# Optimization experiments

Hardware: AMD Instinct MI355X
Metric: run time of the kernel (lower is better)

Reference implementation:

```python
import jax, jax.numpy as jnp
import numpy as np
import math

EMBED_DIM = 1024
N_HEADS = 16
HEAD_DIM = EMBED_DIM // N_HEADS
NUM_FEATURES = 32
R_NODES = 2
EPS = 1e-06
C_CONST = 2.0 + EPS
CHUNK = 512


def setup_inputs() -> dict:
    key = jax.random.key(0)
    ks = jax.random.split(key, 8)
    B, T = 2, 4096
    x = jax.random.normal(ks[0], (B, T, EMBED_DIM), dtype=jnp.float32)
    w_qkv = jax.random.normal(ks[1], (3 * EMBED_DIM, EMBED_DIM), dtype=jnp.float32) * 0.02
    b_qkv = jnp.zeros((3 * EMBED_DIM,), dtype=jnp.float32)
    w_out = jax.random.normal(ks[2], (EMBED_DIM, EMBED_DIM), dtype=jnp.float32) * 0.02
    b_out = jnp.zeros((EMBED_DIM,), dtype=jnp.float32)
    omega = jax.random.normal(ks[3], (R_NODES, N_HEADS, HEAD_DIM, NUM_FEATURES), dtype=jnp.float32)
    nodes, weights = np.polynomial.laguerre.laggauss(R_NODES)
    quad_nodes = jnp.asarray(nodes, dtype=jnp.float32) / C_CONST
    quad_weights = jnp.asarray(weights, dtype=jnp.float32) / C_CONST
    return {"x": x, "w_qkv": w_qkv, "b_qkv": b_qkv, "w_out": w_out,
            "b_out": b_out, "omega": omega, "quad_nodes": quad_nodes,
            "quad_weights": quad_weights}


def _compute_features(z, omega, quad_nodes, quad_weights):
    # z: [B,H,T,D] -> fused features [B,H,T,R*M]
    R, M = omega.shape[0], omega.shape[-1]
    nrm = jnp.linalg.norm(z, axis=-1, keepdims=True)
    zn = z / jnp.maximum(nrm, 1e-12)  # F.normalize
    proj = jnp.einsum('bhtd,rhdm->rbhtm', zn, omega)
    inv_sqrt_m = 1.0 / math.sqrt(M)
    poly = (proj ** 2) * inv_sqrt_m
    s = quad_nodes.reshape(R, 1, 1, 1, 1)
    sqrt_2s = jnp.sqrt(2.0 * jnp.maximum(quad_nodes, 0.0)).reshape(R, 1, 1, 1, 1)
    exp_arg = jnp.clip(proj * sqrt_2s - s, -20.0, 20.0)
    prf = jnp.exp(exp_arg) * inv_sqrt_m
    sqw = jnp.sqrt(jnp.maximum(quad_weights, 0.0)).reshape(R, 1, 1, 1, 1)
    fused = poly * prf * sqw  # [R,B,H,T,M]
    B, H, T = z.shape[0], z.shape[1], z.shape[2]
    return jnp.transpose(fused, (1, 2, 3, 0, 4)).reshape(B, H, T, R * M)


def _forward(x, w_qkv, b_qkv, w_out, b_out, omega, quad_nodes, quad_weights):
    B, T, C = x.shape
    H, D = N_HEADS, HEAD_DIM
    qkv = x @ w_qkv.T + b_qkv  # [B,T,3C]
    q, k, v = jnp.split(qkv, 3, axis=-1)
    def to_bhtd(t):
        return jnp.transpose(t.reshape(B, T, H, D), (0, 2, 1, 3)).astype(jnp.float32)
    q, k, v = to_bhtd(q), to_bhtd(k), to_bhtd(v)
    qf = _compute_features(q, omega, quad_nodes, quad_weights)  # [B,H,T,F]
    kf = _compute_features(k, omega, quad_nodes, quad_weights)
    F_dim = qf.shape[-1]
    nc = T // CHUNK
    # chunked causal linear attention via scan over chunks
    def to_chunks(t):  # [B,H,T,...] -> [nc,B,H,CHUNK,...]
        new_shape = (t.shape[0], t.shape[1], nc, CHUNK) + t.shape[3:]
        return jnp.moveaxis(t.reshape(new_shape), 2, 0)
    qf_c, kf_c, v_c = to_chunks(qf), to_chunks(kf), to_chunks(v)

    kv0 = jnp.zeros((B, H, F_dim, D), dtype=jnp.float32)
    k0 = jnp.zeros((B, H, F_dim), dtype=jnp.float32)

    def step(carry, inp):
        kv_s, k_s = carry
        qc, kc, vc = inp
        kv_prod = jnp.einsum('bhtf,bhtd->bhtfd', kc, vc)
        kv_cum = jnp.cumsum(kv_prod, axis=2) + kv_s[:, :, None]
        k_cum = jnp.cumsum(kc, axis=2) + k_s[:, :, None]
        ctx = jnp.einsum('bhtf,bhtfd->bhtd', qc, kv_cum)
        den = jnp.maximum(jnp.einsum('bhtf,bhtf->bht', qc, k_cum), 1e-06)
        out_c = ctx / den[..., None]
        return (kv_cum[:, :, -1], k_cum[:, :, -1]), out_c

    _, out_chunks = jax.lax.scan(step, (kv0, k0), (qf_c, kf_c, v_c))
    out = jnp.moveaxis(out_chunks, 0, 2).reshape(B, H, T, D)  # [B,H,T,D]
    out = jnp.transpose(out, (0, 2, 1, 3)).reshape(B, T, C)
    return out @ w_out.T + b_out


def reference(x, w_qkv, b_qkv, w_out, b_out, omega, quad_nodes, quad_weights):
    return _forward(x, w_qkv, b_qkv, w_out, b_out, omega, quad_nodes, quad_weights)
```

## Files before the change

kernel.cpp:

```cpp
#include <hip/hip_runtime.h>
#include <math.h>

#define EMBED   1024
#define THREEC  3072
#define NH      16
#define HD      64
#define NFEAT   64
#define RN      2
#define MM_     32
#define B_      2
#define T_      4096
#define L_      64
#define NC_     64
#define BH_     32

typedef __attribute__((ext_vector_type(8))) short bf16x8;
typedef __attribute__((ext_vector_type(4))) short bf16x4;
typedef __attribute__((ext_vector_type(4))) float f32x4;

__device__ __forceinline__ float bf2f(short s) {
    unsigned u = ((unsigned)(unsigned short)s) << 16;
    return __builtin_bit_cast(float, u);
}
__device__ __forceinline__ short f2bf(float f) {
    unsigned u = __builtin_bit_cast(unsigned, f);
    u += 0x7fff + ((u >> 16) & 1);
    return (short)(u >> 16);
}
__device__ __forceinline__ void gload16(const short* g, short* l) {
    __builtin_amdgcn_global_load_lds(
        (const __attribute__((address_space(1))) void*)g,
        (__attribute__((address_space(3))) void*)l, 16, 0, 0);
}

#define NV_X   1048576
#define NV_WQ  393216
#define NV_WO  131072
#define NV_ALL (NV_X + NV_WQ + NV_WO)
__global__ __launch_bounds__(256) void prep_kernel(
    const float* __restrict__ x, const float* __restrict__ wq,
    const float* __restrict__ wo, const float* __restrict__ omega,
    short* __restrict__ xb, short* __restrict__ wqb, short* __restrict__ wob,
    short* __restrict__ omgH, short* __restrict__ omgL)
{
    int i = blockIdx.x * 256 + threadIdx.x;
    if (i < NV_ALL) {
        const float* src; short* dst; int k;
        if (i < NV_X)            { src = x;  dst = xb;  k = i; }
        else if (i < NV_X+NV_WQ) { src = wq; dst = wqb; k = i - NV_X; }
        else                     { src = wo; dst = wob; k = i - NV_X - NV_WQ; }
        const float4* p = (const float4*)src + (size_t)k * 2;
        float4 a = p[0], b = p[1];
        bf16x8 o = { f2bf(a.x), f2bf(a.y), f2bf(a.z), f2bf(a.w),
                     f2bf(b.x), f2bf(b.y), f2bf(b.z), f2bf(b.w) };
        *((bf16x8*)dst + k) = o;
    } else {
        int j = i - NV_ALL;
        if (j < NH * NFEAT * HD) {
            int d = j & 63;
            int f = (j >> 6) & 63;
            int h = j >> 12;
            int r = f >> 5, m = f & 31;
            float w = omega[(((size_t)(r * NH + h) * HD + d) * MM_) + m];
            short a = f2bf(w);
            omgH[j] = a;
            omgL[j] = f2bf(w - bf2f(a));
        }
    }
}

template<int OUTBF>
__global__ __launch_bounds__(256) void gemm_bf16(
    const short* __restrict__ A,
    const short* __restrict__ W,
    const float* __restrict__ bias,
    float* __restrict__ Cf, short* __restrict__ Cb,
    int M, int N, int K)
{
    __shared__ short lA[2][128 * 32];
    __shared__ short lB[2][128 * 32];
    const int tid  = threadIdx.x;
    const int nbn  = N >> 7;
    const int cpx  = gridDim.x >> 3;
    const int swz  = (blockIdx.x & 7) * cpx + (blockIdx.x >> 3);
    const int bm   = (swz / nbn) << 7;
    const int bn   = (swz % nbn) << 7;
    const int lane = tid & 63;
    const int wave = tid >> 6;
    const int row0 = (wave >> 1) * 64;
    const int col0 = (wave & 1) * 64;
    const int lr   = lane & 15;
    const int kg8  = (lane >> 4) * 8;

    f32x4 acc[4][4] = {};

#define STAGE(buf, k0)                                                        \
    {                                                                         \
        _Pragma("unroll")                                                     \
        for (int i = 0; i < 2; ++i) {                                         \
            int idx = i * 256 + tid;                                          \
            int row = idx >> 2, kq = (idx & 3) * 8;                           \
            gload16(&A[(size_t)(bm + row) * K + (k0) + kq], &lA[buf][idx * 8]); \
            gload16(&W[(size_t)(bn + row) * K + (k0) + kq], &lB[buf][idx * 8]); \
        }                                                                     \
    }

    const int KT = K >> 5;
    STAGE(0, 0);
    __syncthreads();
    int cur = 0;
    for (int kt = 0; kt < KT; ++kt) {
        if (kt + 1 < KT) STAGE(cur ^ 1, (kt + 1) * 32);
        const short* As = lA[cur];
        const short* Bs = lB[cur];
        bf16x8 af[4], bfr[4];
        #pragma unroll
        for (int m = 0; m < 4; ++m)
            af[m] = *(const bf16x8*)&As[(row0 + m * 16 + lr) * 32 + kg8];
        #pragma unroll
        for (int n = 0; n < 4; ++n)
            bfr[n] = *(const bf16x8*)&Bs[(col0 + n * 16 + lr) * 32 + kg8];
        #pragma unroll
        for (int m = 0; m < 4; ++m)
            #pragma unroll
            for (int n = 0; n < 4; ++n)
                acc[m][n] = __builtin_amdgcn_mfma_f32_16x16x32_bf16(
                    af[m], bfr[n], acc[m][n], 0, 0, 0);
        __syncthreads();
        cur ^= 1;
    }
#undef STAGE

    #pragma unroll
    for (int n = 0; n < 4; ++n) {
        const int col = bn + col0 + n * 16 + (lane & 15);
        const float bvv = bias[col];
        #pragma unroll
        for (int m = 0; m < 4; ++m) {
            const int rbase = bm + row0 + m * 16 + (lane >> 4) * 4;
            #pragma unroll
            for (int j = 0; j < 4; ++j) {
                const float v = acc[m][n][j] + bvv;
                if (OUTBF) Cb[(size_t)(rbase + j) * N + col] = f2bf(v);
                else       Cf[(size_t)(rbase + j) * N + col] = v;
            }
        }
    }
}

__global__ __launch_bounds__(256) void feat_fused(
    const short* __restrict__ qkvb,
    const short* __restrict__ omgH,
    const short* __restrict__ omgL,
    const float* __restrict__ qn,
    const float* __restrict__ qw,
    short* __restrict__ qf,
    short* __restrict__ ctxb,
    float* __restrict__ rs_g,
    short* __restrict__ cKVb,
    float* __restrict__ cK)
{
    __shared__ short zq[64][72];
    __shared__ short zk[64][72];
    __shared__ short omh[64][72];
    __shared__ short oml[64][72];
    __shared__ float invn[2][64];
    __shared__ float rs_l[64];

    const int tid   = threadIdx.x;
    const int chunk = blockIdx.x;
    const int bh    = chunk >> 6;
    const int c     = chunk & 63;
    const int b     = bh >> 4, h = bh & 15;
    const int t0    = c * 64;

    {
        const int row = tid >> 2;
        const int c0  = (tid & 3) * 16;
        const size_t zbase = ((size_t)(b * T_ + t0 + row)) * THREEC + h * HD + c0;
        const size_t obase = ((size_t)h * NFEAT + row) * HD + c0;
        *(bf16x8*)&zq[row][c0]      = *(const bf16x8*)&qkvb[zbase];
        *(bf16x8*)&zq[row][c0 + 8]  = *(const bf16x8*)&qkvb[zbase + 8];
        *(bf16x8*)&zk[row][c0]      = *(const bf16x8*)&qkvb[zbase + EMBED];
        *(bf16x8*)&zk[row][c0 + 8]  = *(const bf16x8*)&qkvb[zbase + EMBED + 8];
        *(bf16x8*)&omh[row][c0]     = *(const bf16x8*)&omgH[obase];
        *(bf16x8*)&omh[row][c0 + 8] = *(const bf16x8*)&omgH[obase + 8];
        *(bf16x8*)&oml[row][c0]     = *(const bf16x8*)&omgL[obase];
        *(bf16x8*)&oml[row][c0 + 8] = *(const bf16x8*)&omgL[obase + 8];
    }
    __syncthreads();

    {
        const int t = tid >> 2;
        const int q = tid & 3;
        #pragma unroll
        for (int p = 0; p < 2; ++p) {
            const short* Z = p ? &zk[t][q * 16] : &zq[t][q * 16];
            float ss = 0.0f;
            #pragma unroll
            for (int j = 0; j < 16; ++j) { float v = bf2f(Z[j]); ss += v * v; }
            ss += __shfl_xor(ss, 1, 64);
            ss += __shfl_xor(ss, 2, 64);
            if (q == 0) invn[p][t] = 1.0f / fmaxf(sqrtf(ss), 1e-12f);
        }
    }
    __syncthreads();

    const int wave = tid >> 6;
    const int lane = tid & 63;
    const int p    = wave >> 1;
    const int half = wave & 1;
    const short (*Z)[72] = p ? zk : zq;

    const float s0 = qn[0], s1 = qn[1];
    const float sq2s0 = sqrtf(2.0f * fmaxf(s0, 0.0f));
    const float sq2s1 = sqrtf(2.0f * fmaxf(s1, 0.0f));
    const float sc0 = sqrtf(fmaxf(qw[0], 0.0f)) * (1.0f / 32.0f);
    const float sc1 = sqrtf(fmaxf(qw[1], 0.0f)) * (1.0f / 32.0f);

    const int lr  = lane & 15;
    const int G   = lane >> 4;
    const int kg8 = G * 8;

    f32x4 acc[2][4] = {};
    #pragma unroll
    for (int kk = 0; kk < 2; ++kk) {
        bf16x8 a[2], bh8[4], bl8[4];
        #pragma unroll
        for (int m = 0; m < 2; ++m)
            a[m] = *(const bf16x8*)&Z[half * 32 + m * 16 + lr][kk * 32 + kg8];
        #pragma unroll
        for (int n = 0; n < 4; ++n) {
            bh8[n] = *(const bf16x8*)&omh[n * 16 + lr][kk * 32 + kg8];
            bl8[n] = *(const bf16x8*)&oml[n * 16 + lr][kk * 32 + kg8];
        }
        #pragma unroll
        for (int m = 0; m < 2; ++m)
            #pragma unroll
            for (int n = 0; n < 4; ++n) {
                acc[m][n] = __builtin_amdgcn_mfma_f32_16x16x32_bf16(
                    a[m], bh8[n], acc[m][n], 0, 0, 0);
                acc[m][n] = __builtin_amdgcn_mfma_f32_16x16x32_bf16(
                    a[m], bl8[n], acc[m][n], 0, 0, 0);
            }
    }
    __syncthreads();

    short (*kfT)[72] = zq;
    short (*vT)[72]  = zk;
    short (*Qrm)[72] = omh;
    short (*Krm)[72] = oml;
    {
        #pragma unroll
        for (int n = 0; n < 4; ++n) {
            const int f = n * 16 + lr;
            const float s_r   = (n < 2) ? s0 : s1;
            const float sq2s  = (n < 2) ? sq2s0 : sq2s1;
            const float scale = (n < 2) ? sc0 : sc1;
            #pragma unroll
            for (int m = 0; m < 2; ++m) {
                const int tb4 = half * 32 + m * 16 + G * 4;
                #pragma unroll
                for (int j = 0; j < 4; ++j) {
                    const int t = tb4 + j;
                    const float proj = acc[m][n][j] * invn[p][t];
                    const float arg = fminf(fmaxf(proj * sq2s - s_r, -20.0f), 20.0f);
                    const float val = proj * proj * __expf(arg) * scale;
                    const short vb  = f2bf(val);
                    if (p == 0) { Qrm[t][f] = vb; }
                    else        { kfT[f][t] = vb; Krm[t][f] = vb; }
                }
            }
        }
    }
    {
        const int row = tid >> 2;
        const int c0  = (tid & 3) * 16;
        const short* vrow = qkvb + ((size_t)(b * T_ + t0 + row)) * THREEC
                          + 2 * EMBED + h * HD;
        bf16x8 v0 = *(const bf16x8*)&vrow[c0], v1 = *(const bf16x8*)&vrow[c0 + 8];
        #pragma unroll
        for (int j = 0; j < 8; ++j) {
            vT[c0 + j][row]     = v0[j];
            vT[c0 + 8 + j][row] = v1[j];
        }
    }
    __syncthreads();

    const int r0 = wave * 16;

    {
        const int row = tid >> 2;
        const int c0  = (tid & 3) * 16;
        short* dst = qf + ((size_t)bh * T_ + t0 + row) * NFEAT;
        *(bf16x8*)&dst[c0]     = *(const bf16x8*)&Qrm[row][c0];
        *(bf16x8*)&dst[c0 + 8] = *(const bf16x8*)&Qrm[row][c0 + 8];
    }
    bf16x8 aqq[2];
    aqq[0] = *(const bf16x8*)&Qrm[r0 + lr][kg8];
    aqq[1] = *(const bf16x8*)&Qrm[r0 + lr][32 + kg8];
    f32x4 accA[4] = {};
    #pragma unroll
    for (int n = 0; n < 4; ++n) {
        accA[n] = __builtin_amdgcn_mfma_f32_16x16x32_bf16(
            aqq[0], *(const bf16x8*)&Krm[n * 16 + lr][kg8], accA[n], 0, 0, 0);
        accA[n] = __builtin_amdgcn_mfma_f32_16x16x32_bf16(
            aqq[1], *(const bf16x8*)&Krm[n * 16 + lr][32 + kg8], accA[n], 0, 0, 0);
    }
    {
        float rsum[4] = {0.0f, 0.0f, 0.0f, 0.0f};
        #pragma unroll
        for (int n = 0; n < 4; ++n) {
            const int s = n * 16 + lr;
            #pragma unroll
            for (int j = 0; j < 4; ++j) {
                const int t = r0 + G * 4 + j;
                if (s <= t) rsum[j] += accA[n][j];
            }
        }
        #pragma unroll
        for (int j = 0; j < 4; ++j) {
            rsum[j] += __shfl_xor(rsum[j], 1, 64);
            rsum[j] += __shfl_xor(rsum[j], 2, 64);
            rsum[j] += __shfl_xor(rsum[j], 4, 64);
            rsum[j] += __shfl_xor(rsum[j], 8, 64);
        }
        if (lr == 0) {
            #pragma unroll
            for (int j = 0; j < 4; ++j) rs_l[r0 + G * 4 + j] = rsum[j];
        }
    }
    {
        bf16x8 a2[2];
        a2[0] = *(const bf16x8*)&kfT[wave * 16 + lr][kg8];
        a2[1] = *(const bf16x8*)&kfT[wave * 16 + lr][32 + kg8];
        f32x4 sa[4] = {};
        #pragma unroll
        for (int n = 0; n < 4; ++n) {
            sa[n] = __builtin_amdgcn_mfma_f32_16x16x32_bf16(
                a2[0], *(const bf16x8*)&vT[n * 16 + lr][kg8], sa[n], 0, 0, 0);
            sa[n] = __builtin_amdgcn_mfma_f32_16x16x32_bf16(
                a2[1], *(const bf16x8*)&vT[n * 16 + lr][32 + kg8], sa[n], 0, 0, 0);
        }
        short* basep = cKVb + (size_t)chunk * (NFEAT * HD);
        #pragma unroll
        for (int n = 0; n < 4; ++n) {
            bf16x4 o = { f2bf(sa[n][0]), f2bf(sa[n][1]),
                         f2bf(sa[n][2]), f2bf(sa[n][3]) };
            *(bf16x4*)&basep[(n * 16 + lr) * NFEAT + wave * 16 + G * 4] = o;
        }
    }
    {
        const int f  = tid >> 2;
        const int tq = tid & 3;
        float s = 0.0f;
        #pragma unroll
        for (int j = 0; j < 16; ++j) s += bf2f(kfT[f][tq * 16 + j]);
        s += __shfl_xor(s, 1, 64);
        s += __shfl_xor(s, 2, 64);
        if (tq == 0) cK[(size_t)chunk * NFEAT + f] = s;
    }
    __syncthreads();

    short (*At)[72] = oml;
    #pragma unroll
    for (int n = 0; n < 4; ++n) {
        const int s = n * 16 + lr;
        #pragma unroll
        for (int j = 0; j < 4; ++j) {
            const int t = r0 + G * 4 + j;
            At[t][s] = f2bf((s <= t) ? accA[n][j] : 0.0f);
        }
    }
    __syncthreads();

    {
        bf16x8 aa[2];
        aa[0] = *(const bf16x8*)&At[r0 + lr][kg8];
        aa[1] = *(const bf16x8*)&At[r0 + lr][32 + kg8];
        f32x4 a2[4] = {};
        #pragma unroll
        for (int n = 0; n < 4; ++n) {
            a2[n] = __builtin_amdgcn_mfma_f32_16x16x32_bf16(
                aa[0], *(const bf16x8*)&vT[n * 16 + lr][kg8], a2[n], 0, 0, 0);
            a2[n] = __builtin_amdgcn_mfma_f32_16x16x32_bf16(
                aa[1], *(const bf16x8*)&vT[n * 16 + lr][32 + kg8], a2[n], 0, 0, 0);
        }
        #pragma unroll
        for (int n = 0; n < 4; ++n) {
            const int d = n * 16 + lr;
            #pragma unroll
            for (int j = 0; j < 4; ++j) {
                const int t = r0 + G * 4 + j;
                At[t][d] = f2bf(a2[n][j]);
            }
        }
    }
    __syncthreads();
    {
        const int row = tid >> 2;
        const int c0  = (tid & 3) * 16;
        short* dst = ctxb + ((size_t)bh * T_ + t0 + row) * NFEAT;
        *(bf16x8*)&dst[c0]     = *(const bf16x8*)&At[row][c0];
        *(bf16x8*)&dst[c0 + 8] = *(const bf16x8*)&At[row][c0 + 8];
    }
    if (tid < 64) rs_g[(size_t)bh * T_ + t0 + tid] = rs_l[tid];
}

__global__ __launch_bounds__(256) void prefix_scan(
    short* __restrict__ cKVb, float* __restrict__ cK)
{
    const int bh  = blockIdx.x >> 2;
    const int sl  = blockIdx.x & 3;
    const int tid = threadIdx.x;
    short* base = cKVb + (size_t)bh * NC_ * (NFEAT * HD) + sl * 1024 + tid * 4;
    bf16x4 n0 = *(const bf16x4*)(base);
    bf16x4 n1 = *(const bf16x4*)(base + 4096);
    float pref[4] = {0.0f, 0.0f, 0.0f, 0.0f};
    for (int c = 0; c < NC_; ++c) {
        bf16x4 cur = n0;
        n0 = n1;
        if (c + 2 < NC_) n1 = *(const bf16x4*)(base + (size_t)(c + 2) * 4096);
        else { n1[0] = 0; n1[1] = 0; n1[2] = 0; n1[3] = 0; }
        bf16x4 o = { f2bf(pref[0]), f2bf(pref[1]), f2bf(pref[2]), f2bf(pref[3]) };
        *(bf16x4*)(base + (size_t)c * 4096) = o;
        pref[0] += bf2f(cur[0]); pref[1] += bf2f(cur[1]);
        pref[2] += bf2f(cur[2]); pref[3] += bf2f(cur[3]);
    }
    if (sl == 0 && tid < 64) {
        float* kb = cK + (size_t)bh * NC_ * NFEAT + tid;
        float m0 = kb[0];
        float m1 = kb[64];
        float p = 0.0f;
        for (int c = 0; c < NC_; ++c) {
            float cu = m0;
            m0 = m1;
            m1 = (c + 2 < NC_) ? kb[(size_t)(c + 2) * 64] : 0.0f;
            kb[(size_t)c * 64] = p;
            p += cu;
        }
    }
}

__global__ __launch_bounds__(256) void inter_attn(
    const short* __restrict__ qf,
    const short* __restrict__ ctxb,
    const float* __restrict__ rs_g,
    const short* __restrict__ cKVp,
    const float* __restrict__ cKp_g,
    short* __restrict__ attnb)
{
    __shared__ short Q[64][72];
    __shared__ short Pp[64][72];
    __shared__ short Ct[64][72];
    __shared__ float cKp[64], rs[64], qkp_l[64];

    const int tid = threadIdx.x;
    const int chunk = blockIdx.x;
    const int bh = chunk >> 6, c = chunk & 63;
    const int b = bh >> 4, h = bh & 15;
    const int t0 = c * 64;

    {
        const int row = tid >> 2;
        const int c0  = (tid & 3) * 16;
        const short* qrow = qf   + ((size_t)bh * T_ + t0 + row) * NFEAT;
        const short* crow = ctxb + ((size_t)bh * T_ + t0 + row) * NFEAT;
        const short* prow = cKVp + (size_t)chunk * (NFEAT * HD) + row * NFEAT;
        *(bf16x8*)&Q[row][c0]      = *(const bf16x8*)&qrow[c0];
        *(bf16x8*)&Q[row][c0 + 8]  = *(const bf16x8*)&qrow[c0 + 8];
        *(bf16x8*)&Ct[row][c0]     = *(const bf16x8*)&crow[c0];
        *(bf16x8*)&Ct[row][c0 + 8] = *(const bf16x8*)&crow[c0 + 8];
        *(bf16x8*)&Pp[row][c0]     = *(const bf16x8*)&prow[c0];
        *(bf16x8*)&Pp[row][c0 + 8] = *(const bf16x8*)&prow[c0 + 8];
        if (tid < 64) {
            cKp[tid] = cKp_g[(size_t)chunk * NFEAT + tid];
            rs[tid]  = rs_g[(size_t)bh * T_ + t0 + tid];
        }
    }
    __syncthreads();

    {
        const int t  = tid >> 2;
        const int fq = (tid & 3) * 16;
        float s = 0.0f;
        #pragma unroll
        for (int j = 0; j < 16; ++j) s += bf2f(Q[t][fq + j]) * cKp[fq + j];
        s += __shfl_xor(s, 1, 64);
        s += __shfl_xor(s, 2, 64);
        if ((tid & 3) == 0) qkp_l[t] = s;
    }

    const int wave = tid >> 6;
    const int lane = tid & 63;
    const int lr = lane & 15;
    const int G  = lane >> 4;
    const int kg = G * 8;
    const int r0 = wave * 16;

    bf16x8 aq[2];
    aq[0] = *(const bf16x8*)&Q[r0 + lr][kg];
    aq[1] = *(const bf16x8*)&Q[r0 + lr][32 + kg];
    f32x4 acc[4] = {};
    #pragma unroll
    for (int n = 0; n < 4; ++n) {
        acc[n] = __builtin_amdgcn_mfma_f32_16x16x32_bf16(
            aq[0], *(const bf16x8*)&Pp[n * 16 + lr][kg], acc[n], 0, 0, 0);
        acc[n] = __builtin_amdgcn_mfma_f32_16x16x32_bf16(
            aq[1], *(const bf16x8*)&Pp[n * 16 + lr][32 + kg], acc[n], 0, 0, 0);
    }
    __syncthreads();

    float inv[4];
    #pragma unroll
    for (int j = 0; j < 4; ++j) {
        const int t = r0 + G * 4 + j;
        inv[j] = 1.0f / fmaxf(rs[t] + qkp_l[t], 1e-6f);
    }
    #pragma unroll
    for (int n = 0; n < 4; ++n) {
        const int d = n * 16 + lr;
        #pragma unroll
        for (int j = 0; j < 4; ++j) {
            const int t = r0 + G * 4 + j;
            const float ctx = bf2f(Ct[t][d]);
            attnb[((size_t)(b * T_ + t0 + t)) * EMBED + h * HD + d] =
                f2bf((ctx + acc[n][j]) * inv[j]);
        }
    }
}

extern "C" void kernel_launch(void* const* d_in, const int* in_sizes, int n_in,
                              void* d_out, int out_size, void* d_ws, size_t ws_size,
                              hipStream_t stream)
{
    const float* x     = (const float*)d_in[0];
    const float* w_qkv = (const float*)d_in[1];
    const float* b_qkv = (const float*)d_in[2];
    const float* w_out = (const float*)d_in[3];
    const float* b_out = (const float*)d_in[4];
    const float* omega = (const float*)d_in[5];
    const float* qn    = (const float*)d_in[6];
    const float* qw    = (const float*)d_in[7];
    float* out = (float*)d_out;

    short* xb    = (short*)d_ws;
    short* wqb   = xb    + 8388608;
    short* wob   = wqb   + 3145728;
    short* qkvb  = wob   + 1048576;
    short* attnb = qkvb  + 25165824;
    short* omgH  = attnb + 8388608;
    short* omgL  = omgH  + 65536;
    short* qfb   = omgL  + 65536;
    short* ctxb  = qfb   + 8388608;
    short* cKVb  = ctxb  + 8388608;
    float* cK    = (float*)(cKVb + 8388608);
    float* rs_g  = cK + 131072;

    const int M = B_ * T_;

    prep_kernel<<<dim3((NV_ALL + 65536) / 256), 256, 0, stream>>>(
        x, w_qkv, w_out, omega, xb, wqb, wob, omgH, omgL);

    gemm_bf16<1><<<dim3((M / 128) * (THREEC / 128)), 256, 0, stream>>>(
        xb, wqb, b_qkv, nullptr, qkvb, M, THREEC, EMBED);
    feat_fused<<<dim3(BH_ * NC_), 256, 0, stream>>>(
        qkvb, omgH, omgL, qn, qw, qfb, ctxb, rs_g, cKVb, cK);
    prefix_scan<<<dim3(BH_ * 4), 256, 0, stream>>>(cKVb, cK);
    inter_attn<<<dim3(BH_ * NC_), 256, 0, stream>>>(
        qfb, ctxb, rs_g, cKVb, cK, attnb);
    gemm_bf16<0><<<dim3((EMBED / 128) * (M / 128)), 256, 0, stream>>>(
        attnb, wob, b_out, out, nullptr, M, EMBED, EMBED);
}
```

Measured before the change: 169.0 us.

## Fuse feature, prefix-scan and inter-chunk attention into one cooperative kernel

Replaces the three launches (feat_fused, prefix_scan, inter_attn) with a single cooperative kernel that processes two chunks per block and uses grid-wide syncs between phases. Q features and row sums stay in registers across phases, so the qf and rs_g round trips through global memory go away, along with the launch gaps. The cost is grid barriers, and only 128 blocks do the serial prefix scan while the rest wait. If the occupancy check or the cooperative launch fails, it falls back to the old three-kernel path. A missing __syncthreads is also added to the old kernel.

After: 169.5 us. About the same (+0.3%).

```diff
diff --git a/kernel.cpp b/kernel.cpp
--- a/kernel.cpp
+++ b/kernel.cpp
@@ -1,5 +1,8 @@
 #include <hip/hip_runtime.h>
+#include <hip/hip_cooperative_groups.h>
 #include <math.h>
+
+namespace cg = cooperative_groups;
 
 #define EMBED   1024
 #define THREEC  3072
@@ -148,6 +151,366 @@
     }
 }
 
+__global__ __launch_bounds__(256, 4) void mega_attn(
+    const short* __restrict__ qkvb,
+    const short* __restrict__ omgH,
+    const short* __restrict__ omgL,
+    const float* __restrict__ qn,
+    const float* __restrict__ qw,
+    short* __restrict__ ctxb,
+    short* __restrict__ cKVb,
+    float* __restrict__ cK,
+    short* __restrict__ attnb)
+{
+    __shared__ short zq[64][72];
+    __shared__ short zk[64][72];
+    __shared__ short omh[64][72];
+    __shared__ short oml[64][72];
+    __shared__ float invn[2][64];
+
+    const int tid  = threadIdx.x;
+    const int g    = blockIdx.x;
+    const int wave = tid >> 6;
+    const int lane = tid & 63;
+    const int lr   = lane & 15;
+    const int G    = lane >> 4;
+    const int kg8  = G * 8;
+    const int r0   = wave * 16;
+
+    bf16x8 aqR0[2], aqR1[2];
+    float  rsR0[4], rsR1[4];
+
+    #pragma unroll
+    for (int cc = 0; cc < 2; ++cc) {
+        const int chunk = 2 * g + cc;
+        const int bh = chunk >> 6, c = chunk & 63;
+        const int b = bh >> 4, h = bh & 15;
+        const int t0 = c * 64;
+        __syncthreads();
+        {
+            const int row = tid >> 2;
+            const int c0  = (tid & 3) * 16;
+            const size_t zbase = ((size_t)(b * T_ + t0 + row)) * THREEC + h * HD + c0;
+            const size_t obase = ((size_t)h * NFEAT + row) * HD + c0;
+            *(bf16x8*)&zq[row][c0]      = *(const bf16x8*)&qkvb[zbase];
+            *(bf16x8*)&zq[row][c0 + 8]  = *(const bf16x8*)&qkvb[zbase + 8];
+            *(bf16x8*)&zk[row][c0]      = *(const bf16x8*)&qkvb[zbase + EMBED];
+            *(bf16x8*)&zk[row][c0 + 8]  = *(const bf16x8*)&qkvb[zbase + EMBED + 8];
+            *(bf16x8*)&omh[row][c0]     = *(const bf16x8*)&omgH[obase];
+            *(bf16x8*)&omh[row][c0 + 8] = *(const bf16x8*)&omgH[obase + 8];
+            *(bf16x8*)&oml[row][c0]     = *(const bf16x8*)&omgL[obase];
+            *(bf16x8*)&oml[row][c0 + 8] = *(const bf16x8*)&omgL[obase + 8];
+        }
+        __syncthreads();
+        {
+            const int t = tid >> 2;
+            const int q = tid & 3;
+            #pragma unroll
+            for (int p = 0; p < 2; ++p) {
+                const short* Z = p ? &zk[t][q * 16] : &zq[t][q * 16];
+                float ss = 0.0f;
+                #pragma unroll
+                for (int j = 0; j < 16; ++j) { float v = bf2f(Z[j]); ss += v * v; }
+                ss += __shfl_xor(ss, 1, 64);
+                ss += __shfl_xor(ss, 2, 64);
+                if (q == 0) invn[p][t] = 1.0f / fmaxf(sqrtf(ss), 1e-12f);
+            }
+        }
+        __syncthreads();
+
+        const int p    = wave >> 1;
+        const int half = wave & 1;
+        const short (*Z)[72] = p ? zk : zq;
+
+        const float s0 = qn[0], s1 = qn[1];
+        const float sq2s0 = sqrtf(2.0f * fmaxf(s0, 0.0f));
+        const float sq2s1 = sqrtf(2.0f * fmaxf(s1, 0.0f));
+        const float sc0 = sqrtf(fmaxf(qw[0], 0.0f)) * (1.0f / 32.0f);
+        const float sc1 = sqrtf(fmaxf(qw[1], 0.0f)) * (1.0f / 32.0f);
+
+        f32x4 acc[2][4] = {};
+        #pragma unroll
+        for (int kk = 0; kk < 2; ++kk) {
+            bf16x8 a[2], bh8[4], bl8[4];
+            #pragma unroll
+            for (int m = 0; m < 2; ++m)
+                a[m] = *(const bf16x8*)&Z[half * 32 + m * 16 + lr][kk * 32 + kg8];
+            #pragma unroll
+            for (int n = 0; n < 4; ++n) {
+                bh8[n] = *(const bf16x8*)&omh[n * 16 + lr][kk * 32 + kg8];
+                bl8[n] = *(const bf16x8*)&oml[n * 16 + lr][kk * 32 + kg8];
+            }
+            #pragma unroll
+            for (int m = 0; m < 2; ++m)
+                #pragma unroll
+                for (int n = 0; n < 4; ++n) {
+                    acc[m][n] = __builtin_amdgcn_mfma_f32_16x16x32_bf16(
+                        a[m], bh8[n], acc[m][n], 0, 0, 0);
+                    acc[m][n] = __builtin_amdgcn_mfma_f32_16x16x32_bf16(
+                        a[m], bl8[n], acc[m][n], 0, 0, 0);
+                }
+        }
+        __syncthreads();
+
+        short (*kfT)[72] = zq;
+        short (*vT)[72]  = zk;
+        short (*Qrm)[72] = omh;
+        short (*Krm)[72] = oml;
+        {
+            #pragma unroll
+            for (int n = 0; n < 4; ++n) {
+                const int f = n * 16 + lr;
+                const float s_r   = (n < 2) ? s0 : s1;
+                const float sq2s  = (n < 2) ? sq2s0 : sq2s1;
+                const float scale = (n < 2) ? sc0 : sc1;
+                #pragma unroll
+                for (int m = 0; m < 2; ++m) {
+                    const int tb4 = half * 32 + m * 16 + G * 4;
+                    #pragma unroll
+                    for (int j = 0; j < 4; ++j) {
+                        const int t = tb4 + j;
+                        const float proj = acc[m][n][j] * invn[p][t];
+                        const float arg = fminf(fmaxf(proj * sq2s - s_r, -20.0f), 20.0f);
+                        const float val = proj * proj * __expf(arg) * scale;
+                        const short vb  = f2bf(val);
+                        if (p == 0) { Qrm[t][f] = vb; }
+                        else        { kfT[f][t] = vb; Krm[t][f] = vb; }
+                    }
+                }
+            }
+        }
+        {
+            const int row = tid >> 2;
+            const int c0  = (tid & 3) * 16;
+            const short* vrow = qkvb + ((size_t)(b * T_ + t0 + row)) * THREEC
+                              + 2 * EMBED + h * HD;
+            bf16x8 v0 = *(const bf16x8*)&vrow[c0], v1 = *(const bf16x8*)&vrow[c0 + 8];
+            #pragma unroll
+            for (int j = 0; j < 8; ++j) {
+                vT[c0 + j][row]     = v0[j];
+                vT[c0 + 8 + j][row] = v1[j];
+            }
+        }
+        __syncthreads();
+
+        bf16x8 aqq[2];
+        aqq[0] = *(const bf16x8*)&Qrm[r0 + lr][kg8];
+        aqq[1] = *(const bf16x8*)&Qrm[r0 + lr][32 + kg8];
+        if (cc == 0) { aqR0[0] = aqq[0]; aqR0[1] = aqq[1]; }
+        else         { aqR1[0] = aqq[0]; aqR1[1] = aqq[1]; }
+        f32x4 accA[4] = {};
+        #pragma unroll
+        for (int n = 0; n < 4; ++n) {
+            accA[n] = __builtin_amdgcn_mfma_f32_16x16x32_bf16(
+                aqq[0], *(const bf16x8*)&Krm[n * 16 + lr][kg8], accA[n], 0, 0, 0);
+            accA[n] = __builtin_amdgcn_mfma_f32_16x16x32_bf16(
+                aqq[1], *(const bf16x8*)&Krm[n * 16 + lr][32 + kg8], accA[n], 0, 0, 0);
+        }
+        {
+            float rsum[4] = {0.0f, 0.0f, 0.0f, 0.0f};
+            #pragma unroll
+            for (int n = 0; n < 4; ++n) {
+                const int s = n * 16 + lr;
+                #pragma unroll
+                for (int j = 0; j < 4; ++j) {
+                    const int t = r0 + G * 4 + j;
+                    if (s <= t) rsum[j] += accA[n][j];
+                }
+            }
+            #pragma unroll
+            for (int j = 0; j < 4; ++j) {
+                rsum[j] += __shfl_xor(rsum[j], 1, 64);
+                rsum[j] += __shfl_xor(rsum[j], 2, 64);
+                rsum[j] += __shfl_xor(rsum[j], 4, 64);
+                rsum[j] += __shfl_xor(rsum[j], 8, 64);
+            }
+            if (cc == 0) { rsR0[0]=rsum[0]; rsR0[1]=rsum[1]; rsR0[2]=rsum[2]; rsR0[3]=rsum[3]; }
+            else         { rsR1[0]=rsum[0]; rsR1[1]=rsum[1]; rsR1[2]=rsum[2]; rsR1[3]=rsum[3]; }
+        }
+        {
+            bf16x8 a2[2];
+            a2[0] = *(const bf16x8*)&kfT[wave * 16 + lr][kg8];
+            a2[1] = *(const bf16x8*)&kfT[wave * 16 + lr][32 + kg8];
+            f32x4 sa[4] = {};
+            #pragma unroll
+            for (int n = 0; n < 4; ++n) {
+                sa[n] = __builtin_amdgcn_mfma_f32_16x16x32_bf16(
+                    a2[0], *(const bf16x8*)&vT[n * 16 + lr][kg8], sa[n], 0, 0, 0);
+                sa[n] = __builtin_amdgcn_mfma_f32_16x16x32_bf16(
+                    a2[1], *(const bf16x8*)&vT[n * 16 + lr][32 + kg8], sa[n], 0, 0, 0);
+            }
+            short* basep = cKVb + (size_t)chunk * (NFEAT * HD);
+            #pragma unroll
+            for (int n = 0; n < 4; ++n) {
+                bf16x4 o = { f2bf(sa[n][0]), f2bf(sa[n][1]),
+                             f2bf(sa[n][2]), f2bf(sa[n][3]) };
+                *(bf16x4*)&basep[(n * 16 + lr) * NFEAT + wave * 16 + G * 4] = o;
+            }
+        }
+        {
+            const int f  = tid >> 2;
+            const int tq = tid & 3;
+            float s = 0.0f;
+            #pragma unroll
+            for (int j = 0; j < 16; ++j) s += bf2f(kfT[f][tq * 16 + j]);
+            s += __shfl_xor(s, 1, 64);
+            s += __shfl_xor(s, 2, 64);
+            if (tq == 0) cK[(size_t)chunk * NFEAT + f] = s;
+        }
+        __syncthreads();
+
+        short (*At)[72] = oml;
+        #pragma unroll
+        for (int n = 0; n < 4; ++n) {
+            const int s = n * 16 + lr;
+            #pragma unroll
+            for (int j = 0; j < 4; ++j) {
+                const int t = r0 + G * 4 + j;
+                At[t][s] = f2bf((s <= t) ? accA[n][j] : 0.0f);
+            }
+        }
+        __syncthreads();
+        {
+            bf16x8 aa[2];
+            aa[0] = *(const bf16x8*)&At[r0 + lr][kg8];
+            aa[1] = *(const bf16x8*)&At[r0 + lr][32 + kg8];
+            f32x4 a2[4] = {};
+            #pragma unroll
+            for (int n = 0; n < 4; ++n) {
+                a2[n] = __builtin_amdgcn_mfma_f32_16x16x32_bf16(
+                    aa[0], *(const bf16x8*)&vT[n * 16 + lr][kg8], a2[n], 0, 0, 0);
+                a2[n] = __builtin_amdgcn_mfma_f32_16x16x32_bf16(
+                    aa[1], *(const bf16x8*)&vT[n * 16 + lr][32 + kg8], a2[n], 0, 0, 0);
+            }
+            __syncthreads();
+            #pragma unroll
+            for (int n = 0; n < 4; ++n) {
+                const int d = n * 16 + lr;
+                #pragma unroll
+                for (int j = 0; j < 4; ++j) {
+                    const int t = r0 + G * 4 + j;
+                    At[t][d] = f2bf(a2[n][j]);
+                }
+            }
+        }
+        __syncthreads();
+        {
+            const int row = tid >> 2;
+            const int c0  = (tid & 3) * 16;
+            short* dst = ctxb + ((size_t)bh * T_ + t0 + row) * NFEAT;
+            *(bf16x8*)&dst[c0]     = *(const bf16x8*)&At[row][c0];
+            *(bf16x8*)&dst[c0 + 8] = *(const bf16x8*)&At[row][c0 + 8];
+        }
+    }
+
+    __threadfence();
+    cg::this_grid().sync();
+
+    if (g < 128) {
+        const int bh = g >> 2;
+        const int sl = g & 3;
+        short* base = cKVb + (size_t)bh * NC_ * (NFEAT * HD) + sl * 1024 + tid * 4;
+        bf16x4 n0 = *(const bf16x4*)(base);
+        bf16x4 n1 = *(const bf16x4*)(base + 4096);
+        float pref[4] = {0.0f, 0.0f, 0.0f, 0.0f};
+        for (int c = 0; c < NC_; ++c) {
+            bf16x4 cur = n0;
+            n0 = n1;
+            if (c + 2 < NC_) n1 = *(const bf16x4*)(base + (size_t)(c + 2) * 4096);
+            else { n1[0] = 0; n1[1] = 0; n1[2] = 0; n1[3] = 0; }
+            bf16x4 o = { f2bf(pref[0]), f2bf(pref[1]), f2bf(pref[2]), f2bf(pref[3]) };
+            *(bf16x4*)(base + (size_t)c * 4096) = o;
+            pref[0] += bf2f(cur[0]); pref[1] += bf2f(cur[1]);
+            pref[2] += bf2f(cur[2]); pref[3] += bf2f(cur[3]);
+        }
+        if (sl == 0 && tid < 64) {
+            float* kb = cK + (size_t)bh * NC_ * NFEAT + tid;
+            float m0 = kb[0];
+            float m1 = kb[64];
+            float pp = 0.0f;
+            for (int c = 0; c < NC_; ++c) {
+                float cu = m0;
+                m0 = m1;
+                m1 = (c + 2 < NC_) ? kb[(size_t)(c + 2) * 64] : 0.0f;
+                kb[(size_t)c * 64] = pp;
+                pp += cu;
+            }
+        }
+    }
+
+    __threadfence();
+    cg::this_grid().sync();
+    __threadfence();
+
+    #pragma unroll
+    for (int cc = 0; cc < 2; ++cc) {
+        const int chunk = 2 * g + cc;
+        const int bh = chunk >> 6, c = chunk & 63;
+        const int b = bh >> 4, h = bh & 15;
+        const int t0 = c * 64;
+        __syncthreads();
+        {
+            const int row = tid >> 2;
+            const int c0  = (tid & 3) * 16;
+            const short* prow = cKVb + (size_t)chunk * (NFEAT * HD) + row * NFEAT;
+            const short* crow = ctxb + ((size_t)bh * T_ + t0 + row) * NFEAT;
+            *(bf16x8*)&zq[row][c0]     = *(const bf16x8*)&prow[c0];
+            *(bf16x8*)&zq[row][c0 + 8] = *(const bf16x8*)&prow[c0 + 8];
+            *(bf16x8*)&zk[row][c0]     = *(const bf16x8*)&crow[c0];
+            *(bf16x8*)&zk[row][c0 + 8] = *(const bf16x8*)&crow[c0 + 8];
+            if (tid < 64) invn[0][tid] = cK[(size_t)chunk * NFEAT + tid];
+        }
+        __syncthreads();
+
+        const bf16x8 aq0 = cc ? aqR1[0] : aqR0[0];
+        const bf16x8 aq1 = cc ? aqR1[1] : aqR0[1];
+        const float  rsv0 = cc ? rsR1[0] : rsR0[0];
+        const float  rsv1 = cc ? rsR1[1] : rsR0[1];
+        const float  rsv2 = cc ? rsR1[2] : rsR0[2];
+        const float  rsv3 = cc ? rsR1[3] : rsR0[3];
+
+        bf16x8 b0 = {0,0,0,0,0,0,0,0}, b1 = {0,0,0,0,0,0,0,0};
+        if (lr == 0) {
+            #pragma unroll
+            for (int j = 0; j < 8; ++j) {
+                b0[j] = f2bf(invn[0][kg8 + j]);
+                b1[j] = f2bf(invn[0][32 + kg8 + j]);
+            }
+        }
+        f32x4 qk = {};
+        qk = __builtin_amdgcn_mfma_f32_16x16x32_bf16(aq0, b0, qk, 0, 0, 0);
+        qk = __builtin_amdgcn_mfma_f32_16x16x32_bf16(aq1, b1, qk, 0, 0, 0);
+        float qkp[4];
+        #pragma unroll
+        for (int j = 0; j < 4; ++j) qkp[j] = __shfl(qk[j], lane & 48, 64);
+
+        f32x4 acc[4] = {};
+        #pragma unroll
+        for (int n = 0; n < 4; ++n) {
+            acc[n] = __builtin_amdgcn_mfma_f32_16x16x32_bf16(
+                aq0, *(const bf16x8*)&zq[n * 16 + lr][kg8], acc[n], 0, 0, 0);
+            acc[n] = __builtin_amdgcn_mfma_f32_16x16x32_bf16(
+                aq1, *(const bf16x8*)&zq[n * 16 + lr][32 + kg8], acc[n], 0, 0, 0);
+        }
+
+        const float rsv[4] = {rsv0, rsv1, rsv2, rsv3};
+        float inv[4];
+        #pragma unroll
+        for (int j = 0; j < 4; ++j)
+            inv[j] = 1.0f / fmaxf(rsv[j] + qkp[j], 1e-6f);
+        #pragma unroll
+        for (int n = 0; n < 4; ++n) {
+            const int d = n * 16 + lr;
+            #pragma unroll
+            for (int j = 0; j < 4; ++j) {
+                const int t = r0 + G * 4 + j;
+                attnb[((size_t)(b * T_ + t0 + t)) * EMBED + h * HD + d] =
+                    f2bf((bf2f(zk[t][d]) + acc[n][j]) * inv[j]);
+            }
+        }
+    }
+}
+
 __global__ __launch_bounds__(256) void feat_fused(
     const short* __restrict__ qkvb,
     const short* __restrict__ omgH,
@@ -386,6 +749,7 @@
             a2[n] = __builtin_amdgcn_mfma_f32_16x16x32_bf16(
                 aa[1], *(const bf16x8*)&vT[n * 16 + lr][32 + kg8], a2[n], 0, 0, 0);
         }
+        __syncthreads();
         #pragma unroll
         for (int n = 0; n < 4; ++n) {
             const int d = n * 16 + lr;
@@ -564,11 +928,36 @@
 
     gemm_bf16<1><<<dim3((M / 128) * (THREEC / 128)), 256, 0, stream>>>(
         xb, wqb, b_qkv, nullptr, qkvb, M, THREEC, EMBED);
-    feat_fused<<<dim3(BH_ * NC_), 256, 0, stream>>>(
-        qkvb, omgH, omgL, qn, qw, qfb, ctxb, rs_g, cKVb, cK);
-    prefix_scan<<<dim3(BH_ * 4), 256, 0, stream>>>(cKVb, cK);
-    inter_attn<<<dim3(BH_ * NC_), 256, 0, stream>>>(
-        qfb, ctxb, rs_g, cKVb, cK, attnb);
+
+    int maxB = 0;
+    hipError_t qe = hipOccupancyMaxActiveBlocksPerMultiprocessor(
+        &maxB, mega_attn, 256, 0);
+    bool coop_ok = (qe == hipSuccess && maxB >= 4);
+    if (coop_ok) {
+        const short* a_qkvb = qkvb;
+        const short* a_omgH = omgH;
+        const short* a_omgL = omgL;
+        const float* a_qn   = qn;
+        const float* a_qw   = qw;
+        short* a_ctxb  = ctxb;
+        short* a_cKVb  = cKVb;
+        float* a_cK    = cK;
+        short* a_attnb = attnb;
+        void* args[] = { (void*)&a_qkvb, (void*)&a_omgH, (void*)&a_omgL,
+                         (void*)&a_qn, (void*)&a_qw, (void*)&a_ctxb,
+                         (void*)&a_cKVb, (void*)&a_cK, (void*)&a_attnb };
+        hipError_t le = hipLaunchCooperativeKernel(
+            (void*)mega_attn, dim3(BH_ * NC_ / 2), dim3(256), args, 0, stream);
+        if (le != hipSuccess) { (void)hipGetLastError(); coop_ok = false; }
+    }
+    if (!coop_ok) {
+        feat_fused<<<dim3(BH_ * NC_), 256, 0, stream>>>(
+            qkvb, omgH, omgL, qn, qw, qfb, ctxb, rs_g, cKVb, cK);
+        prefix_scan<<<dim3(BH_ * 4), 256, 0, stream>>>(cKVb, cK);
+        inter_attn<<<dim3(BH_ * NC_), 256, 0, stream>>>(
+            qfb, ctxb, rs_g, cKVb, cK, attnb);
+    }
+
     gemm_bf16<0><<<dim3((EMBED / 128) * (M / 128)), 256, 0, stream>>>(
         attnb, wob, b_out, out, nullptr, M, EMBED, EMBED);
 }
```
